# Kernel tuning notes

Measured on AMD Instinct MI355X. Metric: run time of the kernel, lower is better.

Reference implementation:

```python
import jax, jax.numpy as jnp
import numpy as np
from jax import lax

RPN_BBOX_STD_DEV = np.array([0.1, 0.1, 0.2, 0.2], dtype=np.float32)
PRE_NMS_LIMIT = 6000
PROPOSAL_COUNT = 1000
NMS_THRESHOLD = 0.7


def apply_box_deltas(boxes, deltas):
    # boxes: [N,4] (y1,x1,y2,x2); deltas: [N,4] (dy,dx,log dh,log dw)
    h = boxes[:, 2] - boxes[:, 0]
    w = boxes[:, 3] - boxes[:, 1]
    cy = boxes[:, 0] + 0.5 * h + deltas[:, 0] * h
    cx = boxes[:, 1] + 0.5 * w + deltas[:, 1] * w
    h = h * jnp.exp(deltas[:, 2])
    w = w * jnp.exp(deltas[:, 3])
    y1 = cy - 0.5 * h
    x1 = cx - 0.5 * w
    return jnp.stack([y1, x1, y1 + h, x1 + w], axis=1)


def pairwise_iou(boxes):
    # boxes: [N,4] -> iou [N,N]
    y1, x1, y2, x2 = boxes[:, 0], boxes[:, 1], boxes[:, 2], boxes[:, 3]
    area = (y2 - y1) * (x2 - x1)
    iy1 = jnp.maximum(y1[:, None], y1[None, :])
    ix1 = jnp.maximum(x1[:, None], x1[None, :])
    iy2 = jnp.minimum(y2[:, None], y2[None, :])
    ix2 = jnp.minimum(x2[:, None], x2[None, :])
    inter = jnp.maximum(iy2 - iy1, 0.0) * jnp.maximum(ix2 - ix1, 0.0)
    union = area[:, None] + area[None, :] - inter
    return inter / jnp.maximum(union, 1e-12)


def nms_keep_mask(boxes, iou_threshold):
    # boxes are sorted by descending score; greedy suppression.
    n = boxes.shape[0]
    iou = pairwise_iou(boxes)  # [N,N]
    idxs = jnp.arange(n)

    def body(i, keep):
        suppressed = jnp.any((iou[i] > iou_threshold) & keep & (idxs < i))
        return keep.at[i].set(jnp.logical_not(suppressed))

    return lax.fori_loop(0, n, body, jnp.zeros((n,), dtype=bool))


def proposal_single(scores, deltas, anchors):
    # scores: [A], deltas: [A,4], anchors: [A,4] -- single image
    top_scores, ix = lax.top_k(scores, PRE_NMS_LIMIT)           # sorted desc
    d = deltas[ix] * RPN_BBOX_STD_DEV[None, :]
    boxes = apply_box_deltas(anchors[ix], d)
    boxes = jnp.clip(boxes, 0.0, 1.0)                           # window [0,0,1,1]
    keep = lax.stop_gradient(nms_keep_mask(boxes, NMS_THRESHOLD))
    # select top PROPOSAL_COUNT kept boxes in score order, pad with zeros
    masked = jnp.where(keep, top_scores, -jnp.inf)
    _, sel = lax.top_k(masked, PROPOSAL_COUNT)
    valid = keep[sel]
    props = jnp.where(valid[:, None], boxes[sel], 0.0)          # [P,4]
    return props


def reference(rpn_probs, rpn_bbox, anchors):
    scores = rpn_probs[:, :, 1]  # fg prob
    return jax.vmap(proposal_single)(scores, rpn_bbox, anchors)


def setup_inputs() -> dict:
    key = jax.random.key(0)
    k1, k2, k3, k4 = jax.random.split(key, 4)
    B, A = 8, 131072
    rpn_probs = jax.random.uniform(k1, (B, A, 2), dtype=jnp.float32)
    rpn_bbox = jax.random.normal(k2, (B, A, 4), dtype=jnp.float32)
    # valid normalized anchors: y1<y2, x1<x2, inside [0,1]
    tl = jax.random.uniform(k3, (B, A, 2), dtype=jnp.float32) * 0.9
    wh = jax.random.uniform(k4, (B, A, 2), dtype=jnp.float32) * 0.1 + 1e-3
    anchors = jnp.concatenate([tl, tl + wh], axis=-1)
    return {"rpn_probs": rpn_probs, "rpn_bbox": rpn_bbox, "anchors": anchors}
```

## Files before the change

kernel.cpp:

```cpp
#include <hip/hip_runtime.h>

#pragma clang fp contract(off)

typedef unsigned long long u64;
typedef unsigned int u32;
typedef unsigned short u16;

#define BATCH 8
#define NA 131072
#define NSEL 6000
#define NW 94
#define NPAD (NW * 64)
#define CAND_CAP 8192
#define PROP 1000
#define SCAP 1024
#define LDSE 6016
#define CELLCAP 256
#define LARGECAP 1024
#define LTHR 0.125f

#define OFF_HIST     0
#define OFF_BFILL    8256
#define OFF_SCNT     16512
#define OFF_CELLCNT  19584
#define OFF_DIAGT    21696
#define MEMSET_BYTES 406720
#define OFF_CAND     406720
#define OFF_BOXES    931008
#define OFF_CELLLIST 1701056
#define OFF_LARGE    1963200
#define OFF_SENT     1979584

__device__ __forceinline__ int bucket_of(u32 bits) {
  u32 hi = bits >> 16;
  if (hi >= 0x3E80u && hi < 0x3F80u) return (int)(hi - 0x3E80u);
  if (hi >= 0x3F80u && hi < 0x8000u) return 255;
  return -1;
}

__device__ __forceinline__ bool iou_gt(float4 A, float4 B, float areaA, float areaB) {
  float iy = fminf(A.z, B.z) - fmaxf(A.x, B.x);
  float ix = fminf(A.w, B.w) - fmaxf(A.y, B.y);
  float inter = fmaxf(iy, 0.0f) * fmaxf(ix, 0.0f);
  float uni = (areaA + areaB) - inter;
  float uc = fmaxf(uni, 1e-12f);
  return (double)inter >= 0x1.666667p-1 * (double)uc;
}

__device__ __forceinline__ void emit_pair(int b, int ra, int rb, u64* diagT,
                                          u64* sent, int* scnt) {
  int src = min(ra, rb), dst = max(ra, rb);
  int wsrc = src >> 6, wdst = dst >> 6;
  if (wsrc == wdst) {
    atomicOr(&diagT[((size_t)b * NW + wdst) * 64 + (dst & 63)], 1ULL << (src & 63));
  } else {
    int e = atomicAdd(&scnt[b * NW + wsrc], 1);
    if (e < SCAP) {
      u64* p = sent + ((size_t)(b * NW + wsrc) * SCAP + e) * 2;
      p[0] = 1ULL << (dst & 63);
      p[1] = ((u64)(dst >> 6) << 8) | (u64)(src & 63);
    }
  }
}

__device__ __forceinline__ u64 shfl_xor_u64(u64 v, int lanemask) {
  u32 lo = (u32)v, hi = (u32)(v >> 32);
  lo = (u32)__shfl_xor((int)lo, lanemask);
  hi = (u32)__shfl_xor((int)hi, lanemask);
  return ((u64)hi << 32) | (u64)lo;
}

__device__ __forceinline__ void prefix_from_hist(const int* __restrict__ hist, int b,
                                                 int* h, int* bst, int* tb_s) {
  if (threadIdx.x < 256) h[threadIdx.x] = hist[b * 257 + threadIdx.x];
  __syncthreads();
  if (threadIdx.x == 0) {
    int run = 0, t = 0;
    bool found = false;
    for (int v = 255; v >= 0; --v) {
      bst[v] = run;
      run += h[v];
      if (!found && run >= NSEL) { t = v; found = true; }
    }
    *tb_s = t;
  }
  __syncthreads();
}

__global__ __launch_bounds__(256) void hist_kernel(const float* __restrict__ probs,
                                                   int* __restrict__ hist) {
  int b = blockIdx.y;
  __shared__ int h[257];
  for (int i = threadIdx.x; i < 257; i += 256) h[i] = 0;
  __syncthreads();
  int stride = gridDim.x * blockDim.x;
  for (int a = blockIdx.x * blockDim.x + threadIdx.x; a < NA; a += stride) {
    float sc = probs[((size_t)b * NA + a) * 2 + 1];
    int bk = bucket_of(__float_as_uint(sc));
    atomicAdd(&h[bk < 0 ? 256 : bk], 1);
  }
  __syncthreads();
  for (int i = threadIdx.x; i < 257; i += 256)
    if (h[i]) atomicAdd(&hist[b * 257 + i], h[i]);
}

__global__ __launch_bounds__(256) void gather_kernel(const float* __restrict__ probs,
                                                     const int* __restrict__ hist,
                                                     int* __restrict__ bfill,
                                                     u64* __restrict__ cand) {
  int b = blockIdx.y;
  __shared__ int h[256];
  __shared__ int bst[256];
  __shared__ int tb_s;
  prefix_from_hist(hist, b, h, bst, &tb_s);
  int tb = tb_s;
  int stride = gridDim.x * blockDim.x;
  for (int a = blockIdx.x * blockDim.x + threadIdx.x; a < NA; a += stride) {
    float sc = probs[((size_t)b * NA + a) * 2 + 1];
    u32 bits = __float_as_uint(sc);
    int bk = bucket_of(bits);
    if (bk >= tb) {
      int pos = bst[bk] + atomicAdd(&bfill[b * 257 + bk], 1);
      if (pos < CAND_CAP)
        cand[(size_t)b * CAND_CAP + pos] = ((u64)bits << 32) | (u64)(0xFFFFFFFFu - (u32)a);
    }
  }
}

__global__ __launch_bounds__(256) void sortdecode_kernel(const int* __restrict__ hist,
                                                         const int* __restrict__ bfill,
                                                         const u64* __restrict__ cand,
                                                         const float* __restrict__ anchors,
                                                         const float* __restrict__ deltas,
                                                         float4* __restrict__ boxes,
                                                         int* __restrict__ cellCnt,
                                                         u16* __restrict__ cellList,
                                                         u16* __restrict__ largeList) {
  int b = blockIdx.y;
  int tid = threadIdx.x;
  __shared__ int h[256];
  __shared__ int bst[256];
  __shared__ int tb_s;
  prefix_from_hist(hist, b, h, bst, &tb_s);
  if (blockIdx.x == 0) {
    float4 z = {0.f, 0.f, 0.f, 0.f};
    for (int r = NSEL + tid; r < NPAD; r += 256) boxes[(size_t)b * NPAD + r] = z;
  }
  int v = tb_s + blockIdx.x;
  if (v > 255) return;
  int start = bst[v];
  if (start >= NSEL) return;
  int cnt = min(min(bfill[b * 257 + v], 1024), CAND_CAP - start);
  if (cnt <= 0) return;
  const u64* seg = cand + (size_t)b * CAND_CAP + start;
  __shared__ u64 s[1024];
  u64 x[4];
#pragma unroll
  for (int p = 0; p < 4; ++p) {
    int i = p * 256 + tid;
    x[p] = (i < cnt) ? seg[i] : 0ULL;
  }
  for (int k = 2; k <= 64; k <<= 1) {
    for (int j = k >> 1; j >= 1; j >>= 1) {
#pragma unroll
      for (int p = 0; p < 4; ++p) {
        int i = p * 256 + tid;
        u64 pv = shfl_xor_u64(x[p], j);
        bool takemax = (((i & j) == 0) == ((i & k) == 0));
        u64 mx = x[p] > pv ? x[p] : pv;
        u64 mn = x[p] < pv ? x[p] : pv;
        x[p] = takemax ? mx : mn;
      }
    }
  }
#pragma unroll
  for (int p = 0; p < 4; ++p) s[p * 256 + tid] = x[p];
  __syncthreads();
  for (int k = 128; k <= 1024; k <<= 1) {
    for (int j = k >> 1; j >= 64; j >>= 1) {
      for (int q = tid; q < 512; q += 256) {
        int i = ((q & ~(j - 1)) << 1) | (q & (j - 1));
        int ixj = i | j;
        u64 a = s[i], c = s[ixj];
        bool up = ((i & k) == 0);
        if (up ? (a < c) : (a > c)) { s[i] = c; s[ixj] = a; }
      }
      __syncthreads();
    }
#pragma unroll
    for (int p = 0; p < 4; ++p) x[p] = s[p * 256 + tid];
    for (int j = 32; j >= 1; j >>= 1) {
#pragma unroll
      for (int p = 0; p < 4; ++p) {
        int i = p * 256 + tid;
        u64 pv = shfl_xor_u64(x[p], j);
        bool takemax = (((i & j) == 0) == ((i & k) == 0));
        u64 mx = x[p] > pv ? x[p] : pv;
        u64 mn = x[p] < pv ? x[p] : pv;
        x[p] = takemax ? mx : mn;
      }
    }
    __syncthreads();
#pragma unroll
    for (int p = 0; p < 4; ++p) s[p * 256 + tid] = x[p];
    __syncthreads();
  }
  for (int i = tid; i < cnt; i += 256) {
    int r = start + i;
    if (r >= NSEL) continue;
    u64 key = s[i];
    float4 o = {0.f, 0.f, 0.f, 0.f};
    u32 idx = 0xFFFFFFFFu - (u32)(key & 0xFFFFFFFFu);
    if (idx < NA) {
      const float* anc = anchors + ((size_t)b * NA + idx) * 4;
      const float* dl = deltas + ((size_t)b * NA + idx) * 4;
      float y1 = anc[0], x1 = anc[1], y2 = anc[2], x2 = anc[3];
      float dy = dl[0] * 0.1f, dx = dl[1] * 0.1f;
      float dh = dl[2] * 0.2f, dw = dl[3] * 0.2f;
      float hh = y2 - y1, ww = x2 - x1;
      float cy = y1 + 0.5f * hh + dy * hh;
      float cx = x1 + 0.5f * ww + dx * ww;
      hh = hh * expf(dh);
      ww = ww * expf(dw);
      float ny1 = cy - 0.5f * hh, nx1 = cx - 0.5f * ww;
      float ny2 = ny1 + hh, nx2 = nx1 + ww;
      o.x = fminf(fmaxf(ny1, 0.f), 1.f);
      o.y = fminf(fmaxf(nx1, 0.f), 1.f);
      o.z = fminf(fmaxf(ny2, 0.f), 1.f);
      o.w = fminf(fmaxf(nx2, 0.f), 1.f);
    }
    boxes[(size_t)b * NPAD + r] = o;
    float bh = o.z - o.x, bw = o.w - o.y;
    if (bh > LTHR || bw > LTHR) {
      int pos = atomicAdd(&cellCnt[b * 65 + 64], 1);
      if (pos < LARGECAP) largeList[b * LARGECAP + pos] = (u16)r;
    } else {
      int gy = min(7, max(0, (int)((o.x + o.z) * 4.0f)));
      int gx = min(7, max(0, (int)((o.y + o.w) * 4.0f)));
      int cell = gy * 8 + gx;
      int pos = atomicAdd(&cellCnt[b * 65 + cell], 1);
      if (pos < CELLCAP) cellList[((size_t)b * 64 + cell) * CELLCAP + pos] = (u16)r;
    }
  }
}

__global__ __launch_bounds__(256) void pairs_kernel(const float4* __restrict__ boxes,
                                                    const u16* __restrict__ cellList,
                                                    const u16* __restrict__ largeList,
                                                    const int* __restrict__ cellCnt,
                                                    u64* __restrict__ diagT,
                                                    u64* __restrict__ sent,
                                                    int* __restrict__ scnt) {
  int b = blockIdx.y;
  int tid = threadIdx.x;
  if (blockIdx.x >= 64) {
    int lb = blockIdx.x - 64;
    int nL = min(cellCnt[b * 65 + 64], LARGECAP);
    if (nL == 0) return;
    for (int li = lb; li < nL; li += 64) {
      int L = largeList[b * LARGECAP + li];
      float4 Lb = boxes[(size_t)b * NPAD + L];
      float hL = Lb.z - Lb.x, wL = Lb.w - Lb.y;
      if (0.7f * hL >= 0.126f || 0.7f * wL >= 0.126f) continue;
      float La = hL * wL;
      float sLy = Lb.x + Lb.z, sLx = Lb.y + Lb.w;
      int gy0 = max(0, (int)((sLy - 0.08f) * 4.0f));
      int gy1 = min(7, (int)((sLy + 0.08f) * 4.0f));
      int gx0 = max(0, (int)((sLx - 0.08f) * 4.0f));
      int gx1 = min(7, (int)((sLx + 0.08f) * 4.0f));
      for (int gy = gy0; gy <= gy1; ++gy)
        for (int gx = gx0; gx <= gx1; ++gx) {
          int cc = gy * 8 + gx;
          int cnt = min(cellCnt[b * 65 + cc], CELLCAP);
          for (int i = tid; i < cnt; i += 256) {
            int r = cellList[((size_t)b * 64 + cc) * CELLCAP + i];
            float4 jb = boxes[(size_t)b * NPAD + r];
            float ja = (jb.z - jb.x) * (jb.w - jb.y);
            if (iou_gt(Lb, jb, La, ja)) emit_pair(b, L, r, diagT, sent, scnt);
          }
        }
    }
    int s = 1;
    while ((1 << s) < nL) ++s;
    int tot = nL << s, m = (1 << s) - 1;
    int stride = 64 * 256;
    for (int t = lb * 256 + tid; t < tot; t += stride) {
      int i = t >> s, j = t & m;
      if (j >= nL || i >= j) continue;
      int Li = largeList[b * LARGECAP + i];
      int Lj = largeList[b * LARGECAP + j];
      float4 A = boxes[(size_t)b * NPAD + Li];
      float4 B = boxes[(size_t)b * NPAD + Lj];
      float aA = (A.z - A.x) * (A.w - A.y);
      float aB = (B.z - B.x) * (B.w - B.y);
      if (iou_gt(A, B, aA, aB)) emit_pair(b, Li, Lj, diagT, sent, scnt);
    }
    return;
  }
  int c = blockIdx.x;
  int cy = c >> 3, cx = c & 7;
  int nA = min(cellCnt[b * 65 + c], CELLCAP);
  if (nA == 0) return;
  __shared__ float4 Ab[CELLCAP];
  __shared__ float Aa[CELLCAP];
  __shared__ float Asx[CELLCAP];
  __shared__ float Asy[CELLCAP];
  __shared__ u16 Ai[CELLCAP];
  __shared__ u16 fAi[CELLCAP];
  __shared__ float4 Bb[3 * CELLCAP];
  __shared__ float Ba[3 * CELLCAP];
  __shared__ u16 Bi[3 * CELLCAP];
  __shared__ int nfA_s, nfB_s;
  for (int i = tid; i < nA; i += 256) {
    int r = cellList[((size_t)b * 64 + c) * CELLCAP + i];
    float4 bx = boxes[(size_t)b * NPAD + r];
    Ab[i] = bx;
    Aa[i] = (bx.z - bx.x) * (bx.w - bx.y);
    Asy[i] = bx.x + bx.z;
    Asx[i] = bx.y + bx.w;
    Ai[i] = (u16)r;
  }
  __syncthreads();
  {
    int totS = (nA * (nA - 1)) >> 1;
    for (int t = tid; t < totS; t += 256) {
      int i = (int)((1.0f + sqrtf(8.0f * (float)t + 1.0f)) * 0.5f);
      int tri = (i * (i - 1)) >> 1;
      if (t < tri) {
        --i;
        tri = (i * (i - 1)) >> 1;
      } else if (t >= tri + i) {
        tri += i;
        ++i;
      }
      int j = t - tri;
      if (iou_gt(Ab[i], Ab[j], Aa[i], Aa[j]))
        emit_pair(b, Ai[i], Ai[j], diagT, sent, scnt);
    }
  }
  if (cx < 7) {
    __syncthreads();
    if (tid == 0) { nfA_s = 0; nfB_s = 0; }
    __syncthreads();
    float XR2 = (float)(cx + 1) * 0.25f;
    for (int i = tid; i < nA; i += 256)
      if (Asx[i] > XR2 - 0.078f) fAi[atomicAdd(&nfA_s, 1)] = (u16)i;
    int nc = c + 1;
    int nN = min(cellCnt[b * 65 + nc], CELLCAP);
    for (int i = tid; i < nN; i += 256) {
      int r = cellList[((size_t)b * 64 + nc) * CELLCAP + i];
      float4 bx = boxes[(size_t)b * NPAD + r];
      if (bx.y + bx.w < XR2 + 0.078f) {
        int p = atomicAdd(&nfB_s, 1);
        Bb[p] = bx;
        Ba[p] = (bx.z - bx.x) * (bx.w - bx.y);
        Bi[p] = (u16)r;
      }
    }
    __syncthreads();
    int nfA = nfA_s, nfB = nfB_s;
    if (nfA && nfB) {
      int s = 1;
      while ((1 << s) < nfB) ++s;
      int tot = nfA << s, m = (1 << s) - 1;
      for (int t = tid; t < tot; t += 256) {
        int ii = fAi[t >> s], j = t & m;
        if (j < nfB && iou_gt(Ab[ii], Bb[j], Aa[ii], Ba[j]))
          emit_pair(b, Ai[ii], Bi[j], diagT, sent, scnt);
      }
    }
  }
  if (cy < 7) {
    __syncthreads();
    if (tid == 0) { nfA_s = 0; nfB_s = 0; }
    __syncthreads();
    float YB2 = (float)(cy + 1) * 0.25f;
    float XL2 = (float)cx * 0.25f;
    float XR2 = (float)(cx + 1) * 0.25f;
    for (int i = tid; i < nA; i += 256)
      if (Asy[i] > YB2 - 0.078f) fAi[atomicAdd(&nfA_s, 1)] = (u16)i;
    for (int k = 0; k < 3; ++k) {
      int nx = cx + k - 1;
      if (nx < 0 || nx > 7) continue;
      int nc = (cy + 1) * 8 + nx;
      int nN = min(cellCnt[b * 65 + nc], CELLCAP);
      for (int i = tid; i < nN; i += 256) {
        int r = cellList[((size_t)b * 64 + nc) * CELLCAP + i];
        float4 bx = boxes[(size_t)b * NPAD + r];
        float bsy = bx.x + bx.z, bsx = bx.y + bx.w;
        bool ok = bsy < YB2 + 0.078f;
        if (k == 0) ok = ok && (bsx > XL2 - 0.078f);
        if (k == 2) ok = ok && (bsx < XR2 + 0.078f);
        if (ok) {
          int p = atomicAdd(&nfB_s, 1);
          Bb[p] = bx;
          Ba[p] = (bx.z - bx.x) * (bx.w - bx.y);
          Bi[p] = (u16)r;
        }
      }
    }
    __syncthreads();
    int nfA = nfA_s, nfB = nfB_s;
    if (nfA && nfB) {
      int s = 1;
      while ((1 << s) < nfB) ++s;
      int tot = nfA << s, m = (1 << s) - 1;
      for (int t = tid; t < tot; t += 256) {
        int ii = fAi[t >> s], j = t & m;
        if (j < nfB && iou_gt(Ab[ii], Bb[j], Aa[ii], Ba[j]))
          emit_pair(b, Ai[ii], Bi[j], diagT, sent, scnt);
      }
    }
  }
}

__global__ __launch_bounds__(1024) void nms_kernel(const u64* __restrict__ sent,
                                                   const int* __restrict__ scnt,
                                                   const u64* __restrict__ diagT,
                                                   const float4* __restrict__ boxes,
                                                   float4* __restrict__ out) {
  int b = blockIdx.x;
  int tid = threadIdx.x;
  int lane = tid & 63;
  int wv = tid >> 6;
  __shared__ u64 diag_s[NW * 64];
  __shared__ u64 remv[NW];
  __shared__ u64 ebits[LDSE];
  __shared__ u32 emeta[LDSE];
  __shared__ int cw[NW];
  __shared__ int prefix[NW + 1];
  __shared__ u64 Kw[NW];
  __shared__ int baseW[NW];
  for (int i = tid; i < NW * 64; i += 1024)
    diag_s[i] = diagT[(size_t)b * NW * 64 + i];
  if (tid < NW) {
    remv[tid] = 0ULL;
    cw[tid] = min(scnt[b * NW + tid], SCAP);
  }
  __syncthreads();
  if (tid == 0) {
    int run = 0;
    for (int w = 0; w < NW; ++w) { prefix[w] = run; run += cw[w]; }
    prefix[NW] = run;
  }
  __syncthreads();
  for (int w = wv; w < NW; w += 16) {
    const u64* gb = sent + (size_t)(b * NW + w) * SCAP * 2;
    int base = prefix[w], n = cw[w];
    for (int e = lane; e < n; e += 64) {
      int slot = base + e;
      if (slot < LDSE) {
        ebits[slot] = gb[e * 2];
        emeta[slot] = (u32)gb[e * 2 + 1];
      }
    }
  }
  __syncthreads();
  int total = 0;
  for (int w = 0; w < NW; ++w) {
    u64 rm = remv[w];
    u64 cmask = diag_s[w * 64 + lane];
    u64 validm = (w * 64 + 64 <= NSEL) ? ~0ULL : ((1ULL << (NSEL - w * 64)) - 1ULL);
    u64 A0 = ~rm & validm;
    bool alive0 = (A0 >> lane) & 1ULL;
    u64 K = __ballot(alive0);
    for (int it = 0; it < 70; ++it) {
      bool alive = alive0 && ((K & cmask) == 0ULL);
      u64 Kn = __ballot(alive);
      if (Kn == K) break;
      K = Kn;
    }
    if (tid == 0) {
      Kw[w] = K;
      baseW[w] = total;
    }
    total += __popcll(K);
    int base = prefix[w], n = cw[w];
    for (int e = tid; e < n; e += 1024) {
      int slot = base + e;
      u64 bits;
      u32 meta;
      if (slot < LDSE) {
        bits = ebits[slot];
        meta = emeta[slot];
      } else {
        const u64* ge = sent + ((size_t)(b * NW + w) * SCAP + e) * 2;
        bits = ge[0];
        meta = (u32)ge[1];
      }
      int bb = (int)(meta & 255u);
      int fw = (int)(meta >> 8);
      if ((K >> bb) & 1ULL) atomicOr(&remv[fw], bits);
    }
    __syncthreads();
  }
  for (int i = tid; i < NSEL; i += 1024) {
    int w = i >> 6, bb = i & 63;
    u64 K = Kw[w];
    if ((K >> bb) & 1ULL) {
      int rank = baseW[w] + __popcll(K & ((1ULL << bb) - 1ULL));
      if (rank < PROP) out[(size_t)b * PROP + rank] = boxes[(size_t)b * NPAD + i];
    }
  }
}

extern "C" void kernel_launch(void* const* d_in, const int* in_sizes, int n_in,
                              void* d_out, int out_size, void* d_ws, size_t ws_size,
                              hipStream_t stream) {
  const float* probs = (const float*)d_in[0];
  const float* deltas = (const float*)d_in[1];
  const float* anchors = (const float*)d_in[2];
  char* ws = (char*)d_ws;
  int* hist = (int*)(ws + OFF_HIST);
  int* bfill = (int*)(ws + OFF_BFILL);
  int* scnt = (int*)(ws + OFF_SCNT);
  int* cellCnt = (int*)(ws + OFF_CELLCNT);
  u64* diagT = (u64*)(ws + OFF_DIAGT);
  u64* cand = (u64*)(ws + OFF_CAND);
  float4* boxes = (float4*)(ws + OFF_BOXES);
  u16* cellList = (u16*)(ws + OFF_CELLLIST);
  u16* largeList = (u16*)(ws + OFF_LARGE);
  u64* sent = (u64*)(ws + OFF_SENT);

  (void)hipMemsetAsync(ws, 0, MEMSET_BYTES, stream);
  (void)hipMemsetAsync(d_out, 0, (size_t)BATCH * PROP * 4 * sizeof(float), stream);

  hist_kernel<<<dim3(64, BATCH), 256, 0, stream>>>(probs, hist);
  gather_kernel<<<dim3(64, BATCH), 256, 0, stream>>>(probs, hist, bfill, cand);
  sortdecode_kernel<<<dim3(64, BATCH), 256, 0, stream>>>(hist, bfill, cand, anchors,
                                                         deltas, boxes, cellCnt,
                                                         cellList, largeList);
  pairs_kernel<<<dim3(128, BATCH), 256, 0, stream>>>(boxes, cellList, largeList,
                                                     cellCnt, diagT, sent, scnt);
  nms_kernel<<<BATCH, 1024, 0, stream>>>(sent, scnt, diagT, boxes, (float4*)d_out);
}
```

Before: 236.5 us.

## Run NMS serial sweep on a single wavefront and fold output zeroing into kernel

The greedy NMS sweep over 94 word-blocks now runs entirely on wavefront 0. This removes the block-wide __syncthreads per block, with the edge-list atomicOr scatter handled by 64 lanes instead of 1024, and the next diagonal mask is prefetched. Output zeroing moves into the NMS kernel, dropping a separate memset launch. Score, anchor and delta loads are vectorized as float2/float4. The trade-off is less parallelism for the scatter phase in exchange for no barriers.

```diff
diff --git a/kernel.cpp b/kernel.cpp
--- a/kernel.cpp
+++ b/kernel.cpp
@@ -90,12 +90,13 @@
 __global__ __launch_bounds__(256) void hist_kernel(const float* __restrict__ probs,
                                                    int* __restrict__ hist) {
   int b = blockIdx.y;
+  const float2* p2 = reinterpret_cast<const float2*>(probs);
   __shared__ int h[257];
   for (int i = threadIdx.x; i < 257; i += 256) h[i] = 0;
   __syncthreads();
   int stride = gridDim.x * blockDim.x;
   for (int a = blockIdx.x * blockDim.x + threadIdx.x; a < NA; a += stride) {
-    float sc = probs[((size_t)b * NA + a) * 2 + 1];
+    float sc = p2[(size_t)b * NA + a].y;
     int bk = bucket_of(__float_as_uint(sc));
     atomicAdd(&h[bk < 0 ? 256 : bk], 1);
   }
@@ -109,6 +110,7 @@
                                                      int* __restrict__ bfill,
                                                      u64* __restrict__ cand) {
   int b = blockIdx.y;
+  const float2* p2 = reinterpret_cast<const float2*>(probs);
   __shared__ int h[256];
   __shared__ int bst[256];
   __shared__ int tb_s;
@@ -116,7 +118,7 @@
   int tb = tb_s;
   int stride = gridDim.x * blockDim.x;
   for (int a = blockIdx.x * blockDim.x + threadIdx.x; a < NA; a += stride) {
-    float sc = probs[((size_t)b * NA + a) * 2 + 1];
+    float sc = p2[(size_t)b * NA + a].y;
     u32 bits = __float_as_uint(sc);
     int bk = bucket_of(bits);
     if (bk >= tb) {
@@ -212,11 +214,11 @@
     float4 o = {0.f, 0.f, 0.f, 0.f};
     u32 idx = 0xFFFFFFFFu - (u32)(key & 0xFFFFFFFFu);
     if (idx < NA) {
-      const float* anc = anchors + ((size_t)b * NA + idx) * 4;
-      const float* dl = deltas + ((size_t)b * NA + idx) * 4;
-      float y1 = anc[0], x1 = anc[1], y2 = anc[2], x2 = anc[3];
-      float dy = dl[0] * 0.1f, dx = dl[1] * 0.1f;
-      float dh = dl[2] * 0.2f, dw = dl[3] * 0.2f;
+      float4 av = *reinterpret_cast<const float4*>(anchors + ((size_t)b * NA + idx) * 4);
+      float4 dv = *reinterpret_cast<const float4*>(deltas + ((size_t)b * NA + idx) * 4);
+      float y1 = av.x, x1 = av.y, y2 = av.z, x2 = av.w;
+      float dy = dv.x * 0.1f, dx = dv.y * 0.1f;
+      float dh = dv.z * 0.2f, dw = dv.w * 0.2f;
       float hh = y2 - y1, ww = x2 - x1;
       float cy = y1 + 0.5f * hh + dy * hh;
       float cx = x1 + 0.5f * ww + dx * ww;
@@ -437,6 +439,10 @@
     remv[tid] = 0ULL;
     cw[tid] = min(scnt[b * NW + tid], SCAP);
   }
+  {
+    float4 z = {0.f, 0.f, 0.f, 0.f};
+    for (int i = tid; i < PROP; i += 1024) out[(size_t)b * PROP + i] = z;
+  }
   __syncthreads();
   if (tid == 0) {
     int run = 0;
@@ -456,44 +462,48 @@
     }
   }
   __syncthreads();
-  int total = 0;
-  for (int w = 0; w < NW; ++w) {
-    u64 rm = remv[w];
-    u64 cmask = diag_s[w * 64 + lane];
-    u64 validm = (w * 64 + 64 <= NSEL) ? ~0ULL : ((1ULL << (NSEL - w * 64)) - 1ULL);
-    u64 A0 = ~rm & validm;
-    bool alive0 = (A0 >> lane) & 1ULL;
-    u64 K = __ballot(alive0);
-    for (int it = 0; it < 70; ++it) {
-      bool alive = alive0 && ((K & cmask) == 0ULL);
-      u64 Kn = __ballot(alive);
-      if (Kn == K) break;
-      K = Kn;
-    }
-    if (tid == 0) {
-      Kw[w] = K;
-      baseW[w] = total;
-    }
-    total += __popcll(K);
-    int base = prefix[w], n = cw[w];
-    for (int e = tid; e < n; e += 1024) {
-      int slot = base + e;
-      u64 bits;
-      u32 meta;
-      if (slot < LDSE) {
-        bits = ebits[slot];
-        meta = emeta[slot];
-      } else {
-        const u64* ge = sent + ((size_t)(b * NW + w) * SCAP + e) * 2;
-        bits = ge[0];
-        meta = (u32)ge[1];
-      }
-      int bb = (int)(meta & 255u);
-      int fw = (int)(meta >> 8);
-      if ((K >> bb) & 1ULL) atomicOr(&remv[fw], bits);
-    }
-    __syncthreads();
-  }
+  if (wv == 0) {
+    int total = 0;
+    u64 cmask = diag_s[lane];
+    for (int w = 0; w < NW; ++w) {
+      u64 cmask_next = (w + 1 < NW) ? diag_s[(w + 1) * 64 + lane] : 0ULL;
+      u64 rm = remv[w];
+      u64 validm = (w * 64 + 64 <= NSEL) ? ~0ULL : ((1ULL << (NSEL - w * 64)) - 1ULL);
+      u64 A0 = ~rm & validm;
+      bool alive0 = (A0 >> lane) & 1ULL;
+      u64 K = __ballot(alive0);
+      for (int it = 0; it < 70; ++it) {
+        bool alive = alive0 && ((K & cmask) == 0ULL);
+        u64 Kn = __ballot(alive);
+        if (Kn == K) break;
+        K = Kn;
+      }
+      if (lane == 0) {
+        Kw[w] = K;
+        baseW[w] = total;
+      }
+      total += __popcll(K);
+      int base = prefix[w], n = cw[w];
+      for (int e = lane; e < n; e += 64) {
+        int slot = base + e;
+        u64 bits;
+        u32 meta;
+        if (slot < LDSE) {
+          bits = ebits[slot];
+          meta = emeta[slot];
+        } else {
+          const u64* ge = sent + ((size_t)(b * NW + w) * SCAP + e) * 2;
+          bits = ge[0];
+          meta = (u32)ge[1];
+        }
+        int bb = (int)(meta & 255u);
+        int fw = (int)(meta >> 8);
+        if ((K >> bb) & 1ULL) atomicOr(&remv[fw], bits);
+      }
+      cmask = cmask_next;
+    }
+  }
+  __syncthreads();
   for (int i = tid; i < NSEL; i += 1024) {
     int w = i >> 6, bb = i & 63;
     u64 K = Kw[w];
@@ -523,7 +533,6 @@
   u64* sent = (u64*)(ws + OFF_SENT);
 
   (void)hipMemsetAsync(ws, 0, MEMSET_BYTES, stream);
-  (void)hipMemsetAsync(d_out, 0, (size_t)BATCH * PROP * 4 * sizeof(float), stream);
 
   hist_kernel<<<dim3(64, BATCH), 256, 0, stream>>>(probs, hist);
   gather_kernel<<<dim3(64, BATCH), 256, 0, stream>>>(probs, hist, bfill, cand);
```

Result: faster. 231.3 us (-2.2%).
